# Kernel tuning notes

Measured on AMD Instinct MI355X. Metric: run time of the kernel, lower is better.

## Reference

```python
import jax, jax.numpy as jnp
import numpy as np

B, P, D = 8, 576, 1024
H = 16
HD = D // H  # 64
HID = 4 * D  # 4096
EPS = 1e-6  # flax LayerNorm default


def _ln(x, g, b):
    m = jnp.mean(x, axis=-1, keepdims=True)
    v = jnp.var(x, axis=-1, keepdims=True)
    return (x - m) * jax.lax.rsqrt(v + EPS) * g + b


def setup_inputs() -> dict:
    key = jax.random.key(0)
    ks = jax.random.split(key, 8)
    s = 0.02
    return {
        "x": jax.random.normal(ks[0], (B, P, D), dtype=jnp.float32),
        "w_qkv": jax.random.normal(ks[1], (D, 3 * D), dtype=jnp.float32) * s,
        "q_g": jnp.ones((HD,), jnp.float32), "q_b": jnp.zeros((HD,), jnp.float32),
        "k_g": jnp.ones((HD,), jnp.float32), "k_b": jnp.zeros((HD,), jnp.float32),
        "o_g": jnp.ones((D,), jnp.float32), "o_b": jnp.zeros((D,), jnp.float32),
        "w_proj": jax.random.normal(ks[2], (D, D), dtype=jnp.float32) * s,
        "b_proj": jnp.zeros((D,), jnp.float32),
        "ln1_g": jnp.ones((D,), jnp.float32), "ln1_b": jnp.zeros((D,), jnp.float32),
        "ln2_g": jnp.ones((D,), jnp.float32), "ln2_b": jnp.zeros((D,), jnp.float32),
        "w1": jax.random.normal(ks[3], (D, HID), dtype=jnp.float32) * s,
        "b1": jnp.zeros((HID,), jnp.float32),
        "w2": jax.random.normal(ks[4], (HID, D), dtype=jnp.float32) * s,
        "b2": jnp.zeros((D,), jnp.float32),
        "ls1": jnp.full((D,), 1e-5, jnp.float32),
        "ls2": jnp.full((D,), 1e-5, jnp.float32),
    }


def reference(x, w_qkv, q_g, q_b, k_g, k_b, o_g, o_b, w_proj, b_proj,
              ln1_g, ln1_b, ln2_g, ln2_b, w1, b1, w2, b2, ls1, ls2):
    scale = HD ** (-0.5)
    # --- attention branch ---
    o = _ln(x, ln1_g, ln1_b)
    qkv = jnp.einsum('bpd,de->bpe', o, w_qkv)
    qkv = qkv.reshape(B, P, 3, H, HD).transpose(2, 0, 3, 1, 4)  # [3,B,H,P,HD]
    q, k, v = qkv[0], qkv[1], qkv[2]
    q = _ln(q, q_g, q_b) * scale  # QK-LayerNorm per head
    k = _ln(k, k_g, k_b)
    attn = jax.nn.softmax(jnp.einsum('bhqd,bhkd->bhqk', q, k), axis=-1)
    o = jnp.einsum('bhqk,bhkd->bhqd', attn, v)
    o = jnp.swapaxes(o, 1, 2).reshape(B, P, D)
    o = _ln(o, o_g, o_b)
    o = jnp.einsum('bpd,de->bpe', o, w_proj) + b_proj
    x = x + o * ls1
    # --- MLP branch ---
    o = _ln(x, ln2_g, ln2_b)
    o = jax.nn.gelu(jnp.einsum('bpd,dh->bph', o, w1) + b1)  # tanh-approx gelu (flax default)
    o = jnp.einsum('bph,hd->bpd', o, w2) + b2
    return x + o * ls2
```

## Files before the change

### kernel.cpp

```cpp
#include <hip/hip_runtime.h>
#include <hip/hip_bf16.h>

#define DEV static __device__ __forceinline__

typedef short frag8 __attribute__((ext_vector_type(8)));
typedef float accf4 __attribute__((ext_vector_type(4)));


DEV unsigned short f2bf(float f){
  union { float f; unsigned int u; } v; v.f = f;
  unsigned int r = v.u + 0x7fffu + ((v.u >> 16) & 1u);
  return (unsigned short)(r >> 16);
}

DEV void gload16(const void* g, void* l){
  __builtin_amdgcn_global_load_lds((const __attribute__((address_space(1))) void*)g,
                                   (__attribute__((address_space(3))) void*)l, 16, 0, 0);
}

DEV float gelu_tanh(float x){
  float u = 0.7978845608028654f * (x + 0.044715f * x * x * x);
  float e = __expf(2.0f * u);
  float th = 1.0f - 2.0f / (e + 1.0f);
  return 0.5f * x * (1.0f + th);
}

DEV void block_map(int bid, int nwg, int gx, int& tx, int& ty){
  const int swz = ((nwg & 7) == 0) ? ((bid & 7) * (nwg >> 3) + (bid >> 3)) : bid;
  const int gy = nwg / gx;
  const int cg = swz / (gy * 16);
  const int rr = swz - cg * gy * 16;
  const int gw = min(16, gx - cg * 16);
  tx = cg * 16 + rr % gw;
  ty = rr / gw;
}

__global__ __launch_bounds__(256) void wtrans(const float* __restrict__ W,
                                              unsigned short* __restrict__ Wt,
                                              int K, int N){
  __shared__ float t[32][33];
  const int n0 = blockIdx.x * 32, k0 = blockIdx.y * 32;
  const int tx = threadIdx.x, ty = threadIdx.y;
  #pragma unroll
  for (int i = 0; i < 4; i++)
    t[ty + i*8][tx] = W[(long)(k0 + ty + i*8) * N + n0 + tx];
  __syncthreads();
  #pragma unroll
  for (int i = 0; i < 4; i++)
    Wt[(long)(n0 + ty + i*8) * K + k0 + tx] = f2bf(t[tx][ty + i*8]);
}

__global__ __launch_bounds__(256) void ln_rows(const float* __restrict__ in,
                                               const float* __restrict__ g,
                                               const float* __restrict__ beta,
                                               unsigned short* __restrict__ out){
  const long row = blockIdx.x;
  const int t = threadIdx.x;
  const float4 v = ((const float4*)(in + row * 1024))[t];
  float s  = v.x + v.y + v.z + v.w;
  float s2 = v.x*v.x + v.y*v.y + v.z*v.z + v.w*v.w;
  #pragma unroll
  for (int o = 32; o; o >>= 1){ s += __shfl_xor(s, o); s2 += __shfl_xor(s2, o); }
  __shared__ float rs[4], rq[4];
  const int wv = t >> 6;
  if ((t & 63) == 0){ rs[wv] = s; rq[wv] = s2; }
  __syncthreads();
  s  = rs[0] + rs[1] + rs[2] + rs[3];
  s2 = rq[0] + rq[1] + rq[2] + rq[3];
  const float mean = s * (1.f/1024.f);
  const float inv = rsqrtf(s2 * (1.f/1024.f) - mean*mean + 1e-6f);
  const float4 gv = ((const float4*)g)[t];
  const float4 bv = ((const float4*)beta)[t];
  ushort4 o4;
  o4.x = f2bf((v.x - mean)*inv*gv.x + bv.x);
  o4.y = f2bf((v.y - mean)*inv*gv.y + bv.y);
  o4.z = f2bf((v.z - mean)*inv*gv.z + bv.z);
  o4.w = f2bf((v.w - mean)*inv*gv.w + bv.w);
  *(ushort4*)(out + row * 1024 + t * 4) = o4;
}

__global__ __launch_bounds__(256) void v_trans(const float* __restrict__ qkvVf,
                                               unsigned short* __restrict__ Vt){
  const int bh = blockIdx.x, pt = blockIdx.y;
  const int b = bh >> 4, h = bh & 15;
  __shared__ float tile[64][65];
  const int t = threadIdx.x;
  #pragma unroll
  for (int i = 0; i < 16; i++){
    int idx = i * 256 + t; int p = idx >> 6, d = idx & 63;
    tile[p][d] = qkvVf[((long)(b * 576) + pt * 64 + p) * 1024 + h * 64 + d];
  }
  __syncthreads();
  #pragma unroll
  for (int i = 0; i < 16; i++){
    int idx = i * 256 + t; int d = idx >> 6, p = idx & 63;
    Vt[((long)bh * 64 + d) * 576 + pt * 64 + p] = f2bf(tile[p][d]);
  }
}

__global__ __launch_bounds__(256) void attn_k(const unsigned short* __restrict__ Qn,
                                              const unsigned short* __restrict__ Kn,
                                              const unsigned short* __restrict__ Vt,
                                              float* __restrict__ O){
  __shared__ __align__(16) unsigned short Ks[2][4096];
  __shared__ __align__(16) unsigned short Vs[2][4096];
  __shared__ __align__(16) unsigned short Plds[4096];
  const int f = blockIdx.x;
  const int xcd = f & 7, j = f >> 3;
  const int bh = xcd * 16 + j / 9;
  const int qb = j - (j / 9) * 9;
  const int b = bh >> 4, h = bh & 15;
  const int tid = threadIdx.x, w = tid >> 6, l = tid & 63;
  const int fr = l & 15, fq = l >> 4;
  const int rsw = fr & 7;
  const int q0 = qb * 64;

  const unsigned short* qbase = Qn + ((long)bh * 576 + q0 + w * 16 + fr) * 64;
  const frag8 qf0 = *(const frag8*)(qbase + fq * 8);
  const frag8 qf1 = *(const frag8*)(qbase + 32 + fq * 8);

  const int r8 = l >> 3;
  const int kq8 = ((l & 7) ^ r8) * 8;
  const unsigned short* kSrc = Kn + ((long)bh * 576 + w * 16 + r8) * 64 + kq8;
  const unsigned short* vSrc = Vt + ((long)bh * 64 + w * 16 + r8) * 576 + kq8;

  auto stage = [&](int d, int t){
    gload16(kSrc + (long)t * 4096,              &Ks[d][w * 1024]);
    gload16(kSrc + (long)t * 4096 + 512,        &Ks[d][w * 1024 + 512]);
    gload16(vSrc + (long)t * 64,                &Vs[d][w * 1024]);
    gload16(vSrc + (long)t * 64 + 8l * 576,     &Vs[d][w * 1024 + 512]);
  };

  accf4 oacc[4];
  #pragma unroll
  for (int nd = 0; nd < 4; nd++) oacc[nd] = (accf4){0.f, 0.f, 0.f, 0.f};
  float m[4] = {-1e30f, -1e30f, -1e30f, -1e30f};
  float lsum[4] = {0.f, 0.f, 0.f, 0.f};

  stage(0, 0);
  __syncthreads();
  int cur = 0;
  for (int t = 0; t < 9; ++t){
    if (t < 8) stage(cur ^ 1, t + 1);

    accf4 st[4];
    #pragma unroll
    for (int kt4 = 0; kt4 < 4; kt4++){
      const int c0 = ((0 * 4 + fq) ^ rsw) * 8;
      const int c1 = ((1 * 4 + fq) ^ rsw) * 8;
      frag8 kf0 = *(const frag8*)&Ks[cur][(kt4 * 16 + fr) * 64 + c0];
      frag8 kf1 = *(const frag8*)&Ks[cur][(kt4 * 16 + fr) * 64 + c1];
      accf4 a = {0.f, 0.f, 0.f, 0.f};
      a = __builtin_amdgcn_mfma_f32_16x16x32_bf16(qf0, kf0, a, 0, 0, 0);
      a = __builtin_amdgcn_mfma_f32_16x16x32_bf16(qf1, kf1, a, 0, 0, 0);
      st[kt4] = a;
    }

    #pragma unroll
    for (int rr = 0; rr < 4; rr++){
      float v = fmaxf(fmaxf(st[0][rr], st[1][rr]), fmaxf(st[2][rr], st[3][rr]));
      #pragma unroll
      for (int o = 8; o; o >>= 1) v = fmaxf(v, __shfl_xor(v, o));
      const float mn = fmaxf(m[rr], v);
      const float sc = __expf(m[rr] - mn);
      float p[4], rs = 0.f;
      #pragma unroll
      for (int kt4 = 0; kt4 < 4; kt4++){ p[kt4] = __expf(st[kt4][rr] - mn); rs += p[kt4]; }
      #pragma unroll
      for (int o = 8; o; o >>= 1) rs += __shfl_xor(rs, o);
      lsum[rr] = lsum[rr] * sc + rs;
      m[rr] = mn;
      #pragma unroll
      for (int nd = 0; nd < 4; nd++) oacc[nd][rr] *= sc;
      const int prow = fq * 4 + rr;
      #pragma unroll
      for (int kt4 = 0; kt4 < 4; kt4++){
        const int chunk = kt4 * 2 + (fr >> 3);
        Plds[w * 1024 + prow * 64 + ((chunk ^ (prow & 7)) << 3) + (fr & 7)] = f2bf(p[kt4]);
      }
    }

    #pragma unroll
    for (int nd = 0; nd < 4; nd++){
      const int c0 = ((0 * 4 + fq) ^ rsw) * 8;
      const int c1 = ((1 * 4 + fq) ^ rsw) * 8;
      frag8 af0 = *(const frag8*)&Plds[w * 1024 + fr * 64 + c0];
      frag8 af1 = *(const frag8*)&Plds[w * 1024 + fr * 64 + c1];
      frag8 vf0 = *(const frag8*)&Vs[cur][(nd * 16 + fr) * 64 + c0];
      frag8 vf1 = *(const frag8*)&Vs[cur][(nd * 16 + fr) * 64 + c1];
      oacc[nd] = __builtin_amdgcn_mfma_f32_16x16x32_bf16(af0, vf0, oacc[nd], 0, 0, 0);
      oacc[nd] = __builtin_amdgcn_mfma_f32_16x16x32_bf16(af1, vf1, oacc[nd], 0, 0, 0);
    }

    __syncthreads();
    cur ^= 1;
  }

  #pragma unroll
  for (int rr = 0; rr < 4; rr++){
    const float rinv = 1.f / lsum[rr];
    const long orow = (long)b * 576 + q0 + w * 16 + fq * 4 + rr;
    #pragma unroll
    for (int nd = 0; nd < 4; nd++)
      O[orow * 1024 + h * 64 + nd * 16 + fr] = oacc[nd][rr] * rinv;
  }
}

template<int BN, int EPI>
__global__ __launch_bounds__(256) void gemm_bk64(
    const unsigned short* __restrict__ A, const unsigned short* __restrict__ Bt,
    float* __restrict__ Cf, unsigned short* __restrict__ Cb,
    const float* __restrict__ bias, const float* __restrict__ ls,
    const float* __restrict__ resid,
    const float* __restrict__ qg, const float* __restrict__ qb2,
    const float* __restrict__ kg, const float* __restrict__ kb2,
    unsigned short* __restrict__ Qn, unsigned short* __restrict__ Kn,
    float* __restrict__ Vf,
    int M, int N, int K, int gx)
{
  constexpr int NF = BN / 32;
  constexpr int BSLOT = BN / 32;
  __shared__ __align__(16) unsigned short As[2][128 * 64];
  __shared__ __align__(16) unsigned short Bs[2][BN * 64];
  const int tid = threadIdx.x;
  const int wave = tid >> 6, l = tid & 63;
  const int fr = l & 15, fq = l >> 4;
  const int wr = wave >> 1, wc = wave & 1;
  const int rsw = fr & 7;
  int tx, ty;
  block_map(blockIdx.x, gridDim.x, gx, tx, ty);
  const long rowbase = (long)ty * 128;
  const long colbase = (long)tx * BN;

  const int r8 = l >> 3;
  const int kq = (l & 7) ^ r8;
  const unsigned short* aS = A + (rowbase + wave*32 + r8) * (long)K + kq * 8;
  const unsigned short* bS = Bt + (colbase + wave*(BN/4) + r8) * (long)K + kq * 8;

  accf4 acc[4][NF];
  const accf4 zero = {0.f, 0.f, 0.f, 0.f};
  #pragma unroll
  for (int m = 0; m < 4; m++)
    #pragma unroll
    for (int n = 0; n < NF; n++) acc[m][n] = zero;

  auto stage = [&](int d, int t){
    const long k0 = (long)t * 64;
    #pragma unroll
    for (int s = 0; s < 4; s++)
      gload16(aS + (long)s * 8 * K + k0, &As[d][(wave*4 + s) * 512]);
    #pragma unroll
    for (int s = 0; s < BSLOT; s++)
      gload16(bS + (long)s * 8 * K + k0, &Bs[d][(wave*BSLOT + s) * 512]);
  };
  auto compute = [&](int d){
    #pragma unroll
    for (int kk = 0; kk < 2; kk++){
      const int csw = ((kk * 4 + fq) ^ rsw) * 8;
      frag8 bf[NF];
      #pragma unroll
      for (int n = 0; n < NF; n++)
        bf[n] = *(const frag8*)&Bs[d][(wc*(BN/2) + n*16 + fr) * 64 + csw];
      #pragma unroll
      for (int m = 0; m < 4; m++){
        frag8 af = *(const frag8*)&As[d][(wr*64 + m*16 + fr) * 64 + csw];
        #pragma unroll
        for (int n = 0; n < NF; n++)
          acc[m][n] = __builtin_amdgcn_mfma_f32_16x16x32_bf16(af, bf[n], acc[m][n], 0, 0, 0);
      }
    }
  };

  const int NT = K >> 6;
  stage(0, 0);
  __syncthreads();
  int cur = 0;
  for (int t = 0; t < NT; ++t){
    if (t + 1 < NT) stage(cur ^ 1, t + 1);
    compute(cur);
    __syncthreads();
    cur ^= 1;
  }

  if constexpr (EPI == 3){
    const int cg = (int)colbase + wc * 64;
    const int kind = cg >> 10;
    const int h = (cg & 1023) >> 6;
    if (kind < 2){
      const float* g  = kind ? kg : qg;
      const float* bb = kind ? kb2 : qb2;
      const float sc = kind ? 1.0f : 0.125f;
      unsigned short* Out = kind ? Kn : Qn;
      #pragma unroll
      for (int m = 0; m < 4; m++){
        #pragma unroll
        for (int r = 0; r < 4; r++){
          float s1 = 0.f, s2 = 0.f;
          #pragma unroll
          for (int n = 0; n < NF; n++){ const float v = acc[m][n][r]; s1 += v; s2 += v*v; }
          #pragma unroll
          for (int o = 8; o; o >>= 1){ s1 += __shfl_xor(s1, o); s2 += __shfl_xor(s2, o); }
          const float mean = s1 * (1.f/64.f);
          const float inv = rsqrtf(s2 * (1.f/64.f) - mean*mean + 1e-6f);
          const long row = rowbase + wr*64 + m*16 + fq*4 + r;
          const int bq = (int)(row / 576), p = (int)(row - (long)bq*576);
          unsigned short* dst = Out + (((long)(bq*16 + h))*576 + p)*64;
          #pragma unroll
          for (int n = 0; n < NF; n++){
            const int d = n*16 + fr;
            dst[d] = f2bf(((acc[m][n][r] - mean)*inv*g[d] + bb[d]) * sc);
          }
        }
      }
    } else {
      #pragma unroll
      for (int m = 0; m < 4; m++){
        const long rb = rowbase + wr*64 + m*16 + fq*4;
        #pragma unroll
        for (int n = 0; n < NF; n++){
          const int vc = (cg - 2048) + n*16 + fr;
          #pragma unroll
          for (int r = 0; r < 4; r++)
            Vf[(rb + r)*1024 + vc] = acc[m][n][r];
        }
      }
    }
  } else {
    #pragma unroll
    for (int m = 0; m < 4; m++){
      const long rb = rowbase + wr * 64 + m * 16 + fq * 4;
      #pragma unroll
      for (int n = 0; n < NF; n++){
        const long cb = colbase + wc * (BN/2) + n * 16 + fr;
        #pragma unroll
        for (int r = 0; r < 4; r++){
          const long idx = (rb + r) * N + cb;
          const float v = acc[m][n][r];
          if constexpr (EPI == 1){
            Cf[idx] = resid[idx] + (v + bias[cb]) * ls[cb];
          } else {
            Cb[idx] = f2bf(gelu_tanh(v + bias[cb]));
          }
        }
      }
    }
  }
}

extern "C" void kernel_launch(void* const* d_in, const int* in_sizes, int n_in,
                              void* d_out, int out_size, void* d_ws, size_t ws_size,
                              hipStream_t stream){
  (void)in_sizes; (void)n_in; (void)out_size; (void)ws_size;
  const float* x      = (const float*)d_in[0];
  const float* w_qkv  = (const float*)d_in[1];
  const float* q_g    = (const float*)d_in[2];
  const float* q_b    = (const float*)d_in[3];
  const float* k_g    = (const float*)d_in[4];
  const float* k_b    = (const float*)d_in[5];
  const float* o_g    = (const float*)d_in[6];
  const float* o_b    = (const float*)d_in[7];
  const float* w_proj = (const float*)d_in[8];
  const float* b_proj = (const float*)d_in[9];
  const float* ln1_g  = (const float*)d_in[10];
  const float* ln1_b  = (const float*)d_in[11];
  const float* ln2_g  = (const float*)d_in[12];
  const float* ln2_b  = (const float*)d_in[13];
  const float* w1     = (const float*)d_in[14];
  const float* b1     = (const float*)d_in[15];
  const float* w2     = (const float*)d_in[16];
  const float* b2     = (const float*)d_in[17];
  const float* ls1    = (const float*)d_in[18];
  const float* ls2    = (const float*)d_in[19];
  float* out = (float*)d_out;

  char* ws = (char*)d_ws;
  size_t off = 0;
  auto alloc = [&](size_t bytes)->void*{
    void* p = ws + off; off += (bytes + 255) & ~(size_t)255; return p;
  };
  unsigned short* wqkvT  = (unsigned short*)alloc(3072l*1024*2);
  unsigned short* wprojT = (unsigned short*)alloc(1024l*1024*2);
  unsigned short* w1T    = (unsigned short*)alloc(4096l*1024*2);
  unsigned short* w2T    = (unsigned short*)alloc(1024l*4096*2);
  unsigned short* xnA    = (unsigned short*)alloc(4608l*1024*2);
  float*          qkvVf  = (float*)alloc(4608l*1024*4);
  unsigned short* Qn     = (unsigned short*)alloc(73728l*64*2);
  unsigned short* Kn     = (unsigned short*)alloc(73728l*64*2);
  unsigned short* Vt     = (unsigned short*)alloc(73728l*64*2);
  unsigned short* hbf    = (unsigned short*)alloc(4608l*4096*2);
  float*          attnO  = qkvVf;

  wtrans<<<dim3(3072/32, 1024/32), dim3(32,8), 0, stream>>>(w_qkv,  wqkvT,  1024, 3072);
  wtrans<<<dim3(1024/32, 1024/32), dim3(32,8), 0, stream>>>(w_proj, wprojT, 1024, 1024);
  wtrans<<<dim3(4096/32, 1024/32), dim3(32,8), 0, stream>>>(w1,     w1T,    1024, 4096);
  wtrans<<<dim3(1024/32, 4096/32), dim3(32,8), 0, stream>>>(w2,     w2T,    4096, 1024);

  ln_rows<<<4608, 256, 0, stream>>>(x, ln1_g, ln1_b, xnA);
  gemm_bk64<128,3><<<24*36, 256, 0, stream>>>(xnA, wqkvT, nullptr, nullptr,
                                              nullptr, nullptr, nullptr,
                                              q_g, q_b, k_g, k_b, Qn, Kn, qkvVf,
                                              4608, 3072, 1024, 24);
  v_trans<<<dim3(128,9), 256, 0, stream>>>(qkvVf, Vt);
  attn_k<<<1152, 256, 0, stream>>>(Qn, Kn, Vt, attnO);
  ln_rows<<<4608, 256, 0, stream>>>(attnO, o_g, o_b, xnA);
  gemm_bk64<64,1><<<16*36, 256, 0, stream>>>(xnA, wprojT, out, nullptr,
                                             b_proj, ls1, x,
                                             nullptr, nullptr, nullptr, nullptr,
                                             nullptr, nullptr, nullptr,
                                             4608, 1024, 1024, 16);
  ln_rows<<<4608, 256, 0, stream>>>(out, ln2_g, ln2_b, xnA);
  gemm_bk64<64,2><<<64*36, 256, 0, stream>>>(xnA, w1T, nullptr, hbf,
                                             b1, nullptr, nullptr,
                                             nullptr, nullptr, nullptr, nullptr,
                                             nullptr, nullptr, nullptr,
                                             4608, 4096, 1024, 64);
  gemm_bk64<64,1><<<16*36, 256, 0, stream>>>(hbf, w2T, out, nullptr,
                                             b2, ls2, out,
                                             nullptr, nullptr, nullptr, nullptr,
                                             nullptr, nullptr, nullptr,
                                             4608, 1024, 4096, 16);
}
```

Measured before the change: 272.5 us.

## Fuse V transpose into QKV GEMM epilogue and switch QKV GEMM to BN=64

```diff
diff --git a/kernel.cpp b/kernel.cpp
--- a/kernel.cpp
+++ b/kernel.cpp
@@ -79,25 +79,6 @@
   *(ushort4*)(out + row * 1024 + t * 4) = o4;
 }
 
-__global__ __launch_bounds__(256) void v_trans(const float* __restrict__ qkvVf,
-                                               unsigned short* __restrict__ Vt){
-  const int bh = blockIdx.x, pt = blockIdx.y;
-  const int b = bh >> 4, h = bh & 15;
-  __shared__ float tile[64][65];
-  const int t = threadIdx.x;
-  #pragma unroll
-  for (int i = 0; i < 16; i++){
-    int idx = i * 256 + t; int p = idx >> 6, d = idx & 63;
-    tile[p][d] = qkvVf[((long)(b * 576) + pt * 64 + p) * 1024 + h * 64 + d];
-  }
-  __syncthreads();
-  #pragma unroll
-  for (int i = 0; i < 16; i++){
-    int idx = i * 256 + t; int d = idx >> 6, p = idx & 63;
-    Vt[((long)bh * 64 + d) * 576 + pt * 64 + p] = f2bf(tile[p][d]);
-  }
-}
-
 __global__ __launch_bounds__(256) void attn_k(const unsigned short* __restrict__ Qn,
                                               const unsigned short* __restrict__ Kn,
                                               const unsigned short* __restrict__ Vt,
@@ -215,7 +196,7 @@
     const float* __restrict__ qg, const float* __restrict__ qb2,
     const float* __restrict__ kg, const float* __restrict__ kb2,
     unsigned short* __restrict__ Qn, unsigned short* __restrict__ Kn,
-    float* __restrict__ Vf,
+    unsigned short* __restrict__ Vt,
     int M, int N, int K, int gx)
 {
   constexpr int NF = BN / 32;
@@ -283,7 +264,7 @@
   }
 
   if constexpr (EPI == 3){
-    const int cg = (int)colbase + wc * 64;
+    const int cg = (int)colbase;
     const int kind = cg >> 10;
     const int h = (cg & 1023) >> 6;
     if (kind < 2){
@@ -291,23 +272,38 @@
       const float* bb = kind ? kb2 : qb2;
       const float sc = kind ? 1.0f : 0.125f;
       unsigned short* Out = kind ? Kn : Qn;
+      float* part = (float*)&As[0][0];
       #pragma unroll
       for (int m = 0; m < 4; m++){
         #pragma unroll
         for (int r = 0; r < 4; r++){
-          float s1 = 0.f, s2 = 0.f;
-          #pragma unroll
-          for (int n = 0; n < NF; n++){ const float v = acc[m][n][r]; s1 += v; s2 += v*v; }
+          float s1 = acc[m][0][r] + acc[m][1][r];
+          float s2 = acc[m][0][r]*acc[m][0][r] + acc[m][1][r]*acc[m][1][r];
           #pragma unroll
           for (int o = 8; o; o >>= 1){ s1 += __shfl_xor(s1, o); s2 += __shfl_xor(s2, o); }
+          if (fr == 0){
+            const int row = wr*64 + m*16 + fq*4 + r;
+            part[(wc*128 + row)*2]     = s1;
+            part[(wc*128 + row)*2 + 1] = s2;
+          }
+        }
+      }
+      __syncthreads();
+      #pragma unroll
+      for (int m = 0; m < 4; m++){
+        #pragma unroll
+        for (int r = 0; r < 4; r++){
+          const int row = wr*64 + m*16 + fq*4 + r;
+          const float s1 = part[row*2]     + part[(128 + row)*2];
+          const float s2 = part[row*2 + 1] + part[(128 + row)*2 + 1];
           const float mean = s1 * (1.f/64.f);
           const float inv = rsqrtf(s2 * (1.f/64.f) - mean*mean + 1e-6f);
-          const long row = rowbase + wr*64 + m*16 + fq*4 + r;
-          const int bq = (int)(row / 576), p = (int)(row - (long)bq*576);
+          const long grow = rowbase + row;
+          const int bq = (int)(grow / 576), p = (int)(grow - (long)bq*576);
           unsigned short* dst = Out + (((long)(bq*16 + h))*576 + p)*64;
           #pragma unroll
-          for (int n = 0; n < NF; n++){
-            const int d = n*16 + fr;
+          for (int n = 0; n < 2; n++){
+            const int d = wc*32 + n*16 + fr;
             dst[d] = f2bf(((acc[m][n][r] - mean)*inv*g[d] + bb[d]) * sc);
           }
         }
@@ -315,13 +311,15 @@
     } else {
       #pragma unroll
       for (int m = 0; m < 4; m++){
-        const long rb = rowbase + wr*64 + m*16 + fq*4;
+        const long grow = rowbase + wr*64 + m*16 + fq*4;
+        const int bq = (int)(grow / 576), p = (int)(grow - (long)bq*576);
         #pragma unroll
-        for (int n = 0; n < NF; n++){
-          const int vc = (cg - 2048) + n*16 + fr;
-          #pragma unroll
-          for (int r = 0; r < 4; r++)
-            Vf[(rb + r)*1024 + vc] = acc[m][n][r];
+        for (int n = 0; n < 2; n++){
+          const int d = wc*32 + n*16 + fr;
+          ushort4 o4;
+          o4.x = f2bf(acc[m][n][0]); o4.y = f2bf(acc[m][n][1]);
+          o4.z = f2bf(acc[m][n][2]); o4.w = f2bf(acc[m][n][3]);
+          *(ushort4*)(Vt + ((long)(bq*16 + h)*64 + d)*576 + p) = o4;
         }
       }
     }
@@ -383,12 +381,11 @@
   unsigned short* w1T    = (unsigned short*)alloc(4096l*1024*2);
   unsigned short* w2T    = (unsigned short*)alloc(1024l*4096*2);
   unsigned short* xnA    = (unsigned short*)alloc(4608l*1024*2);
-  float*          qkvVf  = (float*)alloc(4608l*1024*4);
   unsigned short* Qn     = (unsigned short*)alloc(73728l*64*2);
   unsigned short* Kn     = (unsigned short*)alloc(73728l*64*2);
   unsigned short* Vt     = (unsigned short*)alloc(73728l*64*2);
   unsigned short* hbf    = (unsigned short*)alloc(4608l*4096*2);
-  float*          attnO  = qkvVf;
+  float*          attnO  = (float*)alloc(4608l*1024*4);
 
   wtrans<<<dim3(3072/32, 1024/32), dim3(32,8), 0, stream>>>(w_qkv,  wqkvT,  1024, 3072);
   wtrans<<<dim3(1024/32, 1024/32), dim3(32,8), 0, stream>>>(w_proj, wprojT, 1024, 1024);
@@ -396,11 +393,10 @@
   wtrans<<<dim3(1024/32, 4096/32), dim3(32,8), 0, stream>>>(w2,     w2T,    4096, 1024);
 
   ln_rows<<<4608, 256, 0, stream>>>(x, ln1_g, ln1_b, xnA);
-  gemm_bk64<128,3><<<24*36, 256, 0, stream>>>(xnA, wqkvT, nullptr, nullptr,
-                                              nullptr, nullptr, nullptr,
-                                              q_g, q_b, k_g, k_b, Qn, Kn, qkvVf,
-                                              4608, 3072, 1024, 24);
-  v_trans<<<dim3(128,9), 256, 0, stream>>>(qkvVf, Vt);
+  gemm_bk64<64,3><<<48*36, 256, 0, stream>>>(xnA, wqkvT, nullptr, nullptr,
+                                             nullptr, nullptr, nullptr,
+                                             q_g, q_b, k_g, k_b, Qn, Kn, Vt,
+                                             4608, 3072, 1024, 48);
   attn_k<<<1152, 256, 0, stream>>>(Qn, Kn, Vt, attnO);
   ln_rows<<<4608, 256, 0, stream>>>(attnO, o_g, o_b, xnA);
   gemm_bk64<64,1><<<16*36, 256, 0, stream>>>(xnA, wprojT, out, nullptr,
```

Result: slower. 279.0 us (+2.4%).
